# Optimization experiments

Measured on AMD Instinct MI355X. Metric: run time of the kernel, lower is better.

## Reference

```python
import jax, jax.numpy as jnp
import numpy as np

N, D_IN, D_OUT, BATCH = 64, 512, 512, 1024


def setup_inputs() -> dict:
    key = jax.random.key(0)
    kx, kw, kb = jax.random.split(key, 3)
    x = jax.random.normal(kx, (BATCH, N, D_IN), dtype=jnp.float32)
    # nn.Linear-style init: U(-1/sqrt(d_in), 1/sqrt(d_in)); weight stored transposed (n, d_in, d_out)
    bound = 1.0 / np.sqrt(D_IN)
    weight = jax.random.uniform(kw, (N, D_IN, D_OUT), minval=-bound, maxval=bound, dtype=jnp.float32)
    bias = jax.random.uniform(kb, (N, D_OUT), minval=-bound, maxval=bound, dtype=jnp.float32)
    return {"x": x, "weight": weight, "bias": bias}


def reference(x, weight, bias):
    # Same math as (x[..., None] * weight[None]).sum(-2) + bias[None],
    # expressed as a batched GEMM over the n independent linear layers.
    out = jnp.einsum("bni,nio->bno", x, weight)  # (batch, n, d_out)
    return out + bias[None]
```

## Files before the change

### kernel.cpp

```cpp
#include <hip/hip_runtime.h>
#include <hip/hip_bf16.h>

#define NL    64
#define DIN   512
#define DOUT  512
#define BATCH 1024

#define BM 128
#define BN 128
#define BK 64
#define NKS (DIN / BK)

typedef short short8 __attribute__((ext_vector_type(8)));
typedef float f32x4  __attribute__((ext_vector_type(4)));

__device__ __forceinline__ unsigned int pk2(float a, float b) {
    __hip_bfloat162 h = __float22bfloat162_rn(make_float2(a, b));
    unsigned int r;
    __builtin_memcpy(&r, &h, 4);
    return r;
}

__global__ __launch_bounds__(256) void wcvt_kernel(
        const float* __restrict__ w, unsigned short* __restrict__ wt) {
    __shared__ float T[64][65];
    const int tid = threadIdx.x;
    const int b   = blockIdx.x;
    const int l   = b >> 6;
    const int kg  = (b >> 3) & 7;
    const int cg  = b & 7;

    const float* src = w + ((size_t)(l * DIN) + kg * 64) * DOUT + cg * 64;
    const int j0 = (tid & 15) * 4;
    const int i0 = tid >> 4;
#pragma unroll
    for (int p = 0; p < 4; ++p) {
        const int i = p * 16 + i0;
        f32x4 v = *reinterpret_cast<const f32x4*>(src + (size_t)i * DOUT + j0);
        T[i][j0] = v[0]; T[i][j0 + 1] = v[1];
        T[i][j0 + 2] = v[2]; T[i][j0 + 3] = v[3];
    }
    __syncthreads();

    const int cl   = tid >> 2;
    const int part = tid & 3;
    const int col  = cg * 64 + cl;
    float v[16];
#pragma unroll
    for (int q = 0; q < 16; ++q) v[q] = T[part * 16 + q][cl];
    uint4 u0, u1;
    u0.x = pk2(v[0], v[1]);  u0.y = pk2(v[2], v[3]);
    u0.z = pk2(v[4], v[5]);  u0.w = pk2(v[6], v[7]);
    u1.x = pk2(v[8], v[9]);  u1.y = pk2(v[10], v[11]);
    u1.z = pk2(v[12], v[13]); u1.w = pk2(v[14], v[15]);
    unsigned short* ob = wt + ((size_t)(l * DOUT) + col) * DIN + kg * 64;
    const int key = col & 7;
    *reinterpret_cast<uint4*>(ob + (((part * 2)     ^ key) << 3)) = u0;
    *reinterpret_cast<uint4*>(ob + (((part * 2 + 1) ^ key) << 3)) = u1;
}

__global__ __launch_bounds__(256, 3) void nlinear_gemm(
        const float* __restrict__ x, const unsigned short* __restrict__ wt,
        const float* __restrict__ bias, float* __restrict__ out) {
    __shared__ float          As[BM * BK];
    __shared__ unsigned short Bs[BN * BK];

    const int tid = threadIdx.x;
    const int bid = blockIdx.x;
    const int nb    = (bid & 7) * 256 + (bid >> 3);
    const int layer = nb >> 5;
    const int tile  = nb & 31;
    const int bm0   = (tile >> 2) * BM;
    const int bn0   = (tile & 3) * BN;

    const int wid  = tid >> 6;
    const int lane = tid & 63;
    const int wr   = wid >> 1, wc = wid & 1;
    const int lrow = lane & 15;
    const int lkb  = lane >> 4;

    const int rowA = tid >> 4;
    const int pA   = tid & 15;
    const int akey = ((rowA & 7) << 1) | ((rowA >> 3) & 1);
    const int colB = tid >> 3;
    const int sB   = tid & 7;

    const size_t XS = (size_t)NL * DIN;
    const float* xb = x + (size_t)bm0 * XS + (size_t)layer * DIN;
    const float* asrc0 = xb + (size_t)rowA * XS + ((pA ^ akey) << 2);
    const unsigned short* bsrc0 =
        wt + ((size_t)(layer * DOUT) + bn0 + colB) * DIN + sB * 8;

    f32x4 acc[4][4];
#pragma unroll
    for (int i = 0; i < 4; ++i)
#pragma unroll
        for (int j = 0; j < 4; ++j) acc[i][j] = (f32x4){0.f, 0.f, 0.f, 0.f};

#pragma unroll 1
    for (int ks = 0; ks < NKS; ++ks) {
        const int k0 = ks * BK;
#pragma unroll
        for (int i = 0; i < 8; ++i) {
            const float* g = asrc0 + (size_t)(i * 16) * XS + k0;
            __builtin_amdgcn_global_load_lds(
                (const __attribute__((address_space(1))) unsigned int*)g,
                (__attribute__((address_space(3))) unsigned int*)
                    ((char*)As + i * 4096 + tid * 16),
                16, 0, 0);
        }
#pragma unroll
        for (int i = 0; i < 4; ++i) {
            const unsigned short* g = bsrc0 + (size_t)(i * 32) * DIN + k0;
            __builtin_amdgcn_global_load_lds(
                (const __attribute__((address_space(1))) unsigned int*)g,
                (__attribute__((address_space(3))) unsigned int*)
                    ((char*)Bs + i * 4096 + tid * 16),
                16, 0, 0);
        }
        __syncthreads();

#pragma unroll
        for (int kk = 0; kk < 2; ++kk) {
            short8 af[4], bf[4];
#pragma unroll
            for (int mi = 0; mi < 4; ++mi) {
                const int row = wr * 64 + mi * 16 + lrow;
                const int key = ((row & 7) << 1) | ((row >> 3) & 1);
                const int sg  = kk * 8 + lkb * 2;
                const float* rp = &As[row * BK];
                f32x4 v0 = *reinterpret_cast<const f32x4*>(rp + ((sg ^ key) << 2));
                f32x4 v1 = *reinterpret_cast<const f32x4*>(rp + (((sg + 1) ^ key) << 2));
                uint4 u;
                u.x = pk2(v0[0], v0[1]); u.y = pk2(v0[2], v0[3]);
                u.z = pk2(v1[0], v1[1]); u.w = pk2(v1[2], v1[3]);
                __builtin_memcpy(&af[mi], &u, 16);
            }
#pragma unroll
            for (int ni = 0; ni < 4; ++ni) {
                const int col = wc * 64 + ni * 16 + lrow;
                const int pos = (kk * 4 + lkb) ^ (col & 7);
                bf[ni] = *reinterpret_cast<const short8*>(&Bs[col * BK + (pos << 3)]);
            }
#pragma unroll
            for (int mi = 0; mi < 4; ++mi)
#pragma unroll
                for (int ni = 0; ni < 4; ++ni)
                    acc[mi][ni] = __builtin_amdgcn_mfma_f32_16x16x32_bf16(
                        af[mi], bf[ni], acc[mi][ni], 0, 0, 0);
        }
        __syncthreads();
    }

    const float* bb = bias + (size_t)layer * DOUT + bn0;
    float* ob = out + (size_t)bm0 * (NL * DOUT) + (size_t)layer * DOUT + bn0;
#pragma unroll
    for (int mi = 0; mi < 4; ++mi) {
#pragma unroll
        for (int ni = 0; ni < 4; ++ni) {
            const int col = wc * 64 + ni * 16 + lrow;
            const float bval = bb[col];
#pragma unroll
            for (int r = 0; r < 4; ++r) {
                const int row = wr * 64 + mi * 16 + lkb * 4 + r;
                ob[(size_t)row * (NL * DOUT) + col] = acc[mi][ni][r] + bval;
            }
        }
    }
}

extern "C" void kernel_launch(void* const* d_in, const int* in_sizes, int n_in,
                              void* d_out, int out_size, void* d_ws, size_t ws_size,
                              hipStream_t stream) {
    const float* x  = (const float*)d_in[0];
    const float* w  = (const float*)d_in[1];
    const float* b  = (const float*)d_in[2];
    float* out      = (float*)d_out;
    unsigned short* wt = (unsigned short*)d_ws;

    hipLaunchKernelGGL(wcvt_kernel, dim3(NL * 8 * 8), dim3(256), 0, stream, w, wt);
    hipLaunchKernelGGL(nlinear_gemm, dim3(NL * (BATCH / BM) * (DOUT / BN)),
                       dim3(256), 0, stream, x, wt, b, out);
}
```

Before: 112.3 us.

## Double-buffer LDS tiles with BK=32 to overlap global loads with MFMA

Halves the K tile to 32 and adds two LDS buffers for A and B, so the next tile's global-to-LDS loads are issued before the current tile's MFMAs run. Each iteration then needs one barrier instead of two. The weight-conversion kernel's swizzle and both LDS swizzles are changed to match the 32-wide rows. In exchange there are twice as many iterations and barriers, each with less compute to hide latency behind, and the explicit waitcnt and sched_barrier calls limit how the compiler can interleave instructions.

```diff
diff --git a/kernel.cpp b/kernel.cpp
--- a/kernel.cpp
+++ b/kernel.cpp
@@ -8,7 +8,7 @@
 
 #define BM 128
 #define BN 128
-#define BK 64
+#define BK 32
 #define NKS (DIN / BK)
 
 typedef short short8 __attribute__((ext_vector_type(8)));
@@ -53,17 +53,19 @@
     u0.z = pk2(v[4], v[5]);  u0.w = pk2(v[6], v[7]);
     u1.x = pk2(v[8], v[9]);  u1.y = pk2(v[10], v[11]);
     u1.z = pk2(v[12], v[13]); u1.w = pk2(v[14], v[15]);
-    unsigned short* ob = wt + ((size_t)(l * DOUT) + col) * DIN + kg * 64;
-    const int key = col & 7;
-    *reinterpret_cast<uint4*>(ob + (((part * 2)     ^ key) << 3)) = u0;
-    *reinterpret_cast<uint4*>(ob + (((part * 2 + 1) ^ key) << 3)) = u1;
+    unsigned short* ob = wt + ((size_t)(l * DOUT) + col) * DIN
+                       + kg * 64 + (part >> 1) * 32;
+    const int key = col & 3;
+    const int s0  = (part & 1) * 2;
+    *reinterpret_cast<uint4*>(ob + ((s0       ^ key) << 3)) = u0;
+    *reinterpret_cast<uint4*>(ob + (((s0 + 1) ^ key) << 3)) = u1;
 }
 
 __global__ __launch_bounds__(256, 3) void nlinear_gemm(
         const float* __restrict__ x, const unsigned short* __restrict__ wt,
         const float* __restrict__ bias, float* __restrict__ out) {
-    __shared__ float          As[BM * BK];
-    __shared__ unsigned short Bs[BN * BK];
+    __shared__ float          As[2][BM * BK];
+    __shared__ unsigned short Bs[2][BN * BK];
 
     const int tid = threadIdx.x;
     const int bid = blockIdx.x;
@@ -79,17 +81,16 @@
     const int lrow = lane & 15;
     const int lkb  = lane >> 4;
 
-    const int rowA = tid >> 4;
-    const int pA   = tid & 15;
-    const int akey = ((rowA & 7) << 1) | ((rowA >> 3) & 1);
-    const int colB = tid >> 3;
-    const int sB   = tid & 7;
+    const int arow  = tid >> 3;
+    const int aoff  = ((tid & 7) ^ (arow & 7)) << 2;
+    const int bcol  = tid >> 2;
+    const int boff  = (tid & 3) * 8;
 
     const size_t XS = (size_t)NL * DIN;
     const float* xb = x + (size_t)bm0 * XS + (size_t)layer * DIN;
-    const float* asrc0 = xb + (size_t)rowA * XS + ((pA ^ akey) << 2);
+    const float* asrc0 = xb + (size_t)arow * XS + aoff;
     const unsigned short* bsrc0 =
-        wt + ((size_t)(layer * DOUT) + bn0 + colB) * DIN + sB * 8;
+        wt + ((size_t)(layer * DOUT) + bn0 + bcol) * DIN + boff;
 
     f32x4 acc[4][4];
 #pragma unroll
@@ -97,59 +98,73 @@
 #pragma unroll
         for (int j = 0; j < 4; ++j) acc[i][j] = (f32x4){0.f, 0.f, 0.f, 0.f};
 
-#pragma unroll 1
-    for (int ks = 0; ks < NKS; ++ks) {
-        const int k0 = ks * BK;
+    auto stage = [&](int t, int db) {
 #pragma unroll
-        for (int i = 0; i < 8; ++i) {
-            const float* g = asrc0 + (size_t)(i * 16) * XS + k0;
+        for (int i = 0; i < 4; ++i) {
+            const float* g = asrc0 + (size_t)(i * 32) * XS + t * BK;
             __builtin_amdgcn_global_load_lds(
                 (const __attribute__((address_space(1))) unsigned int*)g,
                 (__attribute__((address_space(3))) unsigned int*)
-                    ((char*)As + i * 4096 + tid * 16),
+                    ((char*)&As[db][0] + i * 4096 + tid * 16),
                 16, 0, 0);
         }
 #pragma unroll
-        for (int i = 0; i < 4; ++i) {
-            const unsigned short* g = bsrc0 + (size_t)(i * 32) * DIN + k0;
+        for (int i = 0; i < 2; ++i) {
+            const unsigned short* g = bsrc0 + (size_t)(i * 64) * DIN + t * BK;
             __builtin_amdgcn_global_load_lds(
                 (const __attribute__((address_space(1))) unsigned int*)g,
                 (__attribute__((address_space(3))) unsigned int*)
-                    ((char*)Bs + i * 4096 + tid * 16),
+                    ((char*)&Bs[db][0] + i * 4096 + tid * 16),
                 16, 0, 0);
         }
-        __syncthreads();
+    };
+
+    stage(0, 0);
+    asm volatile("s_waitcnt vmcnt(0)" ::: "memory");
+    __builtin_amdgcn_sched_barrier(0);
+    __builtin_amdgcn_s_barrier();
+
+#pragma unroll 1
+    for (int t = 0; t < NKS; ++t) {
+        const int db = t & 1;
+        if (t + 1 < NKS) stage(t + 1, db ^ 1);
+
+        short8 af[4], bf[4];
+#pragma unroll
+        for (int mi = 0; mi < 4; ++mi) {
+            const int row = wr * 64 + mi * 16 + lrow;
+            const int key = row & 7;
+            const float* rp = &As[db][row * BK];
+            f32x4 v0 = *reinterpret_cast<const f32x4*>(
+                rp + (((2 * lkb) ^ key) << 2));
+            f32x4 v1 = *reinterpret_cast<const f32x4*>(
+                rp + (((2 * lkb + 1) ^ key) << 2));
+            uint4 u;
+            u.x = pk2(v0[0], v0[1]); u.y = pk2(v0[2], v0[3]);
+            u.z = pk2(v1[0], v1[1]); u.w = pk2(v1[2], v1[3]);
+            __builtin_memcpy(&af[mi], &u, 16);
+        }
+#pragma unroll
+        for (int ni = 0; ni < 4; ++ni) {
+            const int col = wc * 64 + ni * 16 + lrow;
+            bf[ni] = *reinterpret_cast<const short8*>(
+                &Bs[db][col * BK + ((lkb ^ (col & 3)) << 3)]);
+        }
+        asm volatile("s_waitcnt lgkmcnt(0)" ::: "memory");
+        __builtin_amdgcn_sched_barrier(0);
 
 #pragma unroll
-        for (int kk = 0; kk < 2; ++kk) {
-            short8 af[4], bf[4];
+        for (int mi = 0; mi < 4; ++mi)
 #pragma unroll
-            for (int mi = 0; mi < 4; ++mi) {
-                const int row = wr * 64 + mi * 16 + lrow;
-                const int key = ((row & 7) << 1) | ((row >> 3) & 1);
-                const int sg  = kk * 8 + lkb * 2;
-                const float* rp = &As[row * BK];
-                f32x4 v0 = *reinterpret_cast<const f32x4*>(rp + ((sg ^ key) << 2));
-                f32x4 v1 = *reinterpret_cast<const f32x4*>(rp + (((sg + 1) ^ key) << 2));
-                uint4 u;
-                u.x = pk2(v0[0], v0[1]); u.y = pk2(v0[2], v0[3]);
-                u.z = pk2(v1[0], v1[1]); u.w = pk2(v1[2], v1[3]);
-                __builtin_memcpy(&af[mi], &u, 16);
-            }
-#pragma unroll
-            for (int ni = 0; ni < 4; ++ni) {
-                const int col = wc * 64 + ni * 16 + lrow;
-                const int pos = (kk * 4 + lkb) ^ (col & 7);
-                bf[ni] = *reinterpret_cast<const short8*>(&Bs[col * BK + (pos << 3)]);
-            }
-#pragma unroll
-            for (int mi = 0; mi < 4; ++mi)
-#pragma unroll
-                for (int ni = 0; ni < 4; ++ni)
-                    acc[mi][ni] = __builtin_amdgcn_mfma_f32_16x16x32_bf16(
-                        af[mi], bf[ni], acc[mi][ni], 0, 0, 0);
-        }
-        __syncthreads();
+            for (int ni = 0; ni < 4; ++ni)
+                acc[mi][ni] = __builtin_amdgcn_mfma_f32_16x16x32_bf16(
+                    af[mi], bf[ni], acc[mi][ni], 0, 0, 0);
+
+        if (t + 1 < NKS)
+            asm volatile("s_waitcnt vmcnt(0)" ::: "memory");
+        __builtin_amdgcn_sched_barrier(0);
+        __builtin_amdgcn_s_barrier();
+        __builtin_amdgcn_sched_barrier(0);
     }
 
     const float* bb = bias + (size_t)layer * DOUT + bn0;
```

Measured after the change: 130.0 us. +15.7%, slower.
